# Optimization experiments

Hardware: AMD Instinct MI355X
Metric: run time of the kernel (lower is better)

The kernel has to match this reference:

```python
import jax, jax.numpy as jnp
import numpy as np

B, C, S, D = 16, 32, 64, 512
DFF, E = 2048, 8


def setup_inputs() -> dict:
    key = jax.random.key(0)
    ks = jax.random.split(key, 16)
    std = 0.02
    return {
        'x': jax.random.normal(ks[0], (B, C, S, D), jnp.float32),
        'baseline': jax.random.normal(ks[1], (B, C, S, D), jnp.float32),
        'attnres': jax.random.normal(ks[2], (B, C, S, D), jnp.float32),
        'shared_w1': jax.random.normal(ks[3], (DFF, D), jnp.float32) * std,
        'shared_b1': jnp.zeros((DFF,), jnp.float32),
        'shared_w2': jax.random.normal(ks[4], (D, DFF), jnp.float32) * std,
        'shared_b2': jnp.zeros((D,), jnp.float32),
        'spa_router_w': jax.random.normal(ks[5], (E, 3 * D), jnp.float32) * std,
        'spa_router_b': jnp.zeros((E,), jnp.float32),
        'spe_router_w': jax.random.normal(ks[6], (E, 3 * D), jnp.float32) * std,
        'spe_router_b': jnp.zeros((E,), jnp.float32),
        'spa_w1': jax.random.normal(ks[7], (E, DFF, D), jnp.float32) * std,
        'spa_b1': jnp.zeros((E, DFF), jnp.float32),
        'spa_w2': jax.random.normal(ks[8], (E, D, DFF), jnp.float32) * std,
        'spa_b2': jnp.zeros((E, D), jnp.float32),
        'spe_w1': jax.random.normal(ks[9], (E, DFF, D), jnp.float32) * std,
        'spe_b1': jnp.zeros((E, DFF), jnp.float32),
        'spe_w2': jax.random.normal(ks[10], (E, D, DFF), jnp.float32) * std,
        'spe_b2': jnp.zeros((E, D), jnp.float32),
    }


def _route(feat, rw, rb):
    # feat [B, 3D] -> top-1 expert index [B] and its softmax gate weight [B]
    logits = feat @ rw.T + rb            # [B, E]
    p = jax.nn.softmax(logits, axis=-1)
    idx = jnp.argmax(logits, axis=-1)    # [B]
    w = jnp.take_along_axis(p, idx[:, None], axis=-1)[:, 0]
    return idx, w


def _specialist(xf, idx, w1, b1, w2, b2):
    # xf [B, T, D]; per-sample gather of expert weights then batched FFN
    W1, B1 = w1[idx], b1[idx]            # [B, DFF, D], [B, DFF]
    W2, B2 = w2[idx], b2[idx]            # [B, D, DFF], [B, D]
    h = jax.nn.gelu(jnp.einsum('btd,bfd->btf', xf, W1) + B1[:, None, :])
    return jnp.einsum('btf,bdf->btd', h, W2) + B2[:, None, :]


def reference(x, baseline, attnres, shared_w1, shared_b1, shared_w2, shared_b2,
              spa_router_w, spa_router_b, spe_router_w, spe_router_b,
              spa_w1, spa_b1, spa_w2, spa_b2, spe_w1, spe_b1, spe_w2, spe_b2):
    b, d = x.shape[0], x.shape[-1]
    xf = x.reshape(b, -1, d)  # [B, T, D]
    # sample-level AttnRes router features: [B, 3*d_model]
    feat = jnp.concatenate([
        baseline.mean(axis=(1, 2)),
        attnres.mean(axis=(1, 2)),
        (attnres - baseline).mean(axis=(1, 2)),
    ], axis=-1)
    spa_idx, spa_w = _route(feat, spa_router_w, spa_router_b)
    spe_idx, spe_w = _route(feat, spe_router_w, spe_router_b)
    # shared dense FFN (dropout=0 eval)
    shared = jax.nn.gelu(xf @ shared_w1.T + shared_b1) @ shared_w2.T + shared_b2
    spa_out = _specialist(xf, spa_idx, spa_w1, spa_b1, spa_w2, spa_b2)
    spe_out = _specialist(xf, spe_idx, spe_w1, spe_b1, spe_w2, spe_b2)
    y = shared + spa_w[:, None, None] * spa_out + spe_w[:, None, None] * spe_out
    return y.reshape(x.shape)
```

## Files before the change

kernel.cpp:

```cpp
#include <hip/hip_runtime.h>
#include <cstdint>
#include <cstddef>

#define DEV __device__ __forceinline__

typedef unsigned short u16;
typedef _Float16 f16x8 __attribute__((ext_vector_type(8)));
typedef float f32x4 __attribute__((ext_vector_type(4)));

static constexpr int NB  = 16;
static constexpr int T   = 2048;
static constexpr int D   = 512;
static constexpr int DFF = 2048;
static constexpr int NE  = 8;
static constexpr int FEAT = 3 * D;

#define MFMA16 __builtin_amdgcn_mfma_f32_16x16x32_f16

DEV u16 f2h(float f) {
  _Float16 h = (_Float16)f;
  union { _Float16 h; u16 u; } cv; cv.h = h; return cv.u;
}

DEV float gelu_fast(float x) {
  const float t = x * x;
  const float p = x * fmaf(t, -0.07135481627f, -1.59576912161f);
  return __fdividef(x, 1.0f + __expf(p));
}


__global__ void k_part(const float* __restrict__ base, const float* __restrict__ attn,
                       float* __restrict__ part) {
  const int b = blockIdx.x >> 4, ch = blockIdx.x & 15;
  const int d = threadIdx.x;
  const size_t o = ((size_t)b * T + (size_t)ch * 128) * D + d;
  const float* pb = base + o;
  const float* pa = attn + o;
  float sb = 0.f, sa = 0.f;
  for (int r = 0; r < 128; ++r) { sb += pb[(size_t)r * D]; sa += pa[(size_t)r * D]; }
  part[(b * 16 + ch) * D + d] = sb;
  part[NB * 16 * D + (b * 16 + ch) * D + d] = sa;
}

__global__ void k_feat(const float* __restrict__ part, float* __restrict__ feat) {
  const int b = blockIdx.x, d = threadIdx.x;
  float sb = 0.f, sa = 0.f;
  for (int ch = 0; ch < 16; ++ch) {
    sb += part[(b * 16 + ch) * D + d];
    sa += part[NB * 16 * D + (b * 16 + ch) * D + d];
  }
  sb *= (1.0f / 2048.0f); sa *= (1.0f / 2048.0f);
  feat[b * FEAT + d] = sb;
  feat[b * FEAT + D + d] = sa;
  feat[b * FEAT + 2 * D + d] = sa - sb;
}

__global__ void k_route(const float* __restrict__ feat,
                        const float* __restrict__ rw0, const float* __restrict__ rb0,
                        const float* __restrict__ rw1, const float* __restrict__ rb1,
                        int* __restrict__ idx, float* __restrict__ gate) {
  const int r = blockIdx.x >> 4, b = blockIdx.x & 15;
  const float* rw = (r == 0) ? rw0 : rw1;
  const float* rb = (r == 0) ? rb0 : rb1;
  const int l = threadIdx.x;
  float p[8];
#pragma unroll
  for (int e = 0; e < 8; ++e) p[e] = 0.f;
  const float* f = feat + b * FEAT;
  for (int k = l; k < FEAT; k += 64) {
    const float fv = f[k];
#pragma unroll
    for (int e = 0; e < 8; ++e) p[e] += fv * rw[e * FEAT + k];
  }
#pragma unroll
  for (int off = 32; off >= 1; off >>= 1) {
#pragma unroll
    for (int e = 0; e < 8; ++e) p[e] += __shfl_xor(p[e], off);
  }
  if (l == 0) {
    float best = -1e30f; int bi = 0;
    float lg[8];
#pragma unroll
    for (int e = 0; e < 8; ++e) {
      lg[e] = p[e] + rb[e];
      if (lg[e] > best) { best = lg[e]; bi = e; }
    }
    float s = 0.f;
#pragma unroll
    for (int e = 0; e < 8; ++e) s += expf(lg[e] - best);
    idx[r * 16 + b] = bi;
    gate[r * 16 + b] = 1.0f / s;
  }
}

__global__ void k_btot(const float* __restrict__ b2s, const float* __restrict__ b2a,
                       const float* __restrict__ b2e, const int* __restrict__ idx,
                       const float* __restrict__ gate, float* __restrict__ btot) {
  const int b = blockIdx.x, d = threadIdx.x;
  const int ia = idx[b], ie = idx[16 + b];
  const float ga = gate[b], ge = gate[16 + b];
  btot[b * D + d] = b2s[d] + ga * b2a[ia * D + d] + ge * b2e[ie * D + d];
}

__global__ void k_cast(const float* __restrict__ s, u16* __restrict__ d, long n) {
  const long i = ((long)blockIdx.x * blockDim.x + threadIdx.x) * 4;
  if (i >= n) return;
  const float4 v = *(const float4*)(s + i);
  const unsigned int lo = (unsigned int)f2h(v.x) | ((unsigned int)f2h(v.y) << 16);
  const unsigned int hi = (unsigned int)f2h(v.z) | ((unsigned int)f2h(v.w) << 16);
  *(uint2*)(d + i) = make_uint2(lo, hi);
}


DEV void ld_lds16(const void* g, void* l) {
  __builtin_amdgcn_global_load_lds((const __attribute__((address_space(1))) void*)g,
                                   (__attribute__((address_space(3))) void*)l, 16, 0, 0);
}

template <int NC>
DEV void gemm_pipe(const u16* __restrict__ A, int lda, const u16* __restrict__ B, int ldb,
                   u16* As, u16* Bs, f32x4 (&acc)[8][4]) {
  static_assert(NC >= 4, "pipeline needs >=4 chunks");
  const int tid = threadIdx.x;
  const int lane = tid & 63, wid = tid >> 6;
  const int wr = wid >> 2, wc = wid & 3;

  const int r0 = wid * 32 + (lane >> 2);
  const int r1 = r0 + 16;
  const int cb0 = (lane & 3) ^ ((r0 >> 1) & 3);
  const int cb1 = (lane & 3) ^ ((r1 >> 1) & 3);
  const int ldsO0 = wid * 1024;
  const int ldsO1 = wid * 1024 + 512;
  const u16* gA0 = A + (size_t)r0 * lda + cb0 * 8;
  const u16* gA1 = A + (size_t)r1 * lda + cb1 * 8;
  const u16* gB0 = B + (size_t)r0 * ldb + cb0 * 8;
  const u16* gB1 = B + (size_t)r1 * ldb + cb1 * 8;

  const int kb = lane >> 4;
  int ar[8], br[4];
#pragma unroll
  for (int m = 0; m < 8; ++m) {
    const int R = wr * 128 + m * 16 + (lane & 15);
    ar[m] = R * 64 + ((kb ^ ((R >> 1) & 3)) * 16);
  }
#pragma unroll
  for (int n = 0; n < 4; ++n) {
    const int C = wc * 64 + n * 16 + (lane & 15);
    br[n] = C * 64 + ((kb ^ ((C >> 1) & 3)) * 16);
  }

  {
    const u16 *a0 = gA0, *a1 = gA1, *b0 = gB0, *b1 = gB1;
#pragma unroll
    for (int c = 0; c < 3; ++c) {
      ld_lds16(a0, As + c * 8192 + ldsO0);
      ld_lds16(a1, As + c * 8192 + ldsO1);
      ld_lds16(b0, Bs + c * 8192 + ldsO0);
      ld_lds16(b1, Bs + c * 8192 + ldsO1);
      a0 += 32; a1 += 32; b0 += 32; b1 += 32;
    }
  }
  const u16 *sA0 = gA0 + 96, *sA1 = gA1 + 96, *sB0 = gB0 + 96, *sB1 = gB1 + 96;
  asm volatile("s_waitcnt vmcnt(8)" ::: "memory");
  __builtin_amdgcn_s_barrier();

  for (int ch = 0; ch < NC; ++ch) {
    const char* Asl = (const char*)(As + (ch & 3) * 8192);
    const char* Bsl = (const char*)(Bs + (ch & 3) * 8192);
    const bool st = (ch + 3) < NC;
    const int ssl = (ch + 3) & 3;

    f16x8 av[8], bv0, bv1, bv2, bv3;
#pragma unroll
    for (int m = 0; m < 8; ++m) av[m] = *(const f16x8*)(Asl + ar[m]);
    bv0 = *(const f16x8*)(Bsl + br[0]);
    bv1 = *(const f16x8*)(Bsl + br[1]);
    if (st) {
      ld_lds16(sA0, As + ssl * 8192 + ldsO0);
      ld_lds16(sA1, As + ssl * 8192 + ldsO1);
    }
    __builtin_amdgcn_s_barrier();
    asm volatile("s_waitcnt lgkmcnt(0)" ::: "memory");
    __builtin_amdgcn_s_setprio(1);
#pragma unroll
    for (int m = 0; m < 8; ++m) {
      acc[m][0] = MFMA16(av[m], bv0, acc[m][0], 0, 0, 0);
      acc[m][1] = MFMA16(av[m], bv1, acc[m][1], 0, 0, 0);
    }
    __builtin_amdgcn_s_setprio(0);
    __builtin_amdgcn_s_barrier();

    bv2 = *(const f16x8*)(Bsl + br[2]);
    bv3 = *(const f16x8*)(Bsl + br[3]);
    if (st) {
      ld_lds16(sB0, Bs + ssl * 8192 + ldsO0);
      ld_lds16(sB1, Bs + ssl * 8192 + ldsO1);
    }
    __builtin_amdgcn_s_barrier();
    asm volatile("s_waitcnt lgkmcnt(0)" ::: "memory");
    __builtin_amdgcn_s_setprio(1);
#pragma unroll
    for (int m = 0; m < 8; ++m) {
      acc[m][2] = MFMA16(av[m], bv2, acc[m][2], 0, 0, 0);
      acc[m][3] = MFMA16(av[m], bv3, acc[m][3], 0, 0, 0);
    }
    __builtin_amdgcn_s_setprio(0);
    sA0 += 32; sA1 += 32; sB0 += 32; sB1 += 32;

    if (ch < NC - 3)       asm volatile("s_waitcnt vmcnt(8)" ::: "memory");
    else if (ch == NC - 3) asm volatile("s_waitcnt vmcnt(4)" ::: "memory");
    else if (ch == NC - 2) asm volatile("s_waitcnt vmcnt(0)" ::: "memory");
    __builtin_amdgcn_s_barrier();
  }
}

template <int BANK>
__global__ __launch_bounds__(512, 2) void k_ffn1(
    const u16* __restrict__ xh, const u16* __restrict__ w1, const float* __restrict__ b1,
    const int* __restrict__ idx, const float* __restrict__ gate, u16* __restrict__ h) {
  __shared__ alignas(16) u16 As[4 * 8192];
  __shared__ alignas(16) u16 Bs[4 * 8192];
  int wg = blockIdx.x;
  const int q = (int)gridDim.x >> 3;
  wg = (wg & 7) * q + (wg >> 3);
  const int b  = wg >> 6;
  const int mt = (wg >> 3) & 7;
  const int nt = wg & 7;

  const int e   = (BANK == 0) ? 0 : idx[(BANK - 1) * 16 + b];
  const float g = (BANK == 0) ? 1.0f : gate[(BANK - 1) * 16 + b];
  const u16* Ab = xh + ((size_t)b * T + (size_t)mt * 256) * D;
  const u16* Bb = w1 + (size_t)e * DFF * D + (size_t)nt * 256 * D;
  const float* bb = b1 + (size_t)e * DFF;

  f32x4 acc[8][4];
#pragma unroll
  for (int m = 0; m < 8; ++m)
#pragma unroll
    for (int n = 0; n < 4; ++n)
#pragma unroll
      for (int r = 0; r < 4; ++r) acc[m][n][r] = 0.f;

  gemm_pipe<16>(Ab, D, Bb, D, As, Bs, acc);

  const int lane = threadIdx.x & 63, wid = threadIdx.x >> 6;
  const int wr = wid >> 2, wc = wid & 3;
  const int rr = (lane >> 4) << 2, cc = lane & 15;
  const int mrow = mt * 256 + wr * 128;
  const int ncol = nt * 256 + wc * 64;
  u16* hb = h + (size_t)b * T * DFF;
  float bias[4];
#pragma unroll
  for (int n = 0; n < 4; ++n) bias[n] = bb[ncol + n * 16 + cc];
#pragma unroll
  for (int m = 0; m < 8; ++m) {
    const int row = mrow + m * 16 + rr;
#pragma unroll
    for (int n = 0; n < 4; ++n) {
      const int col = ncol + n * 16 + cc;
      const f32x4 a = acc[m][n];
#pragma unroll
      for (int r = 0; r < 4; ++r) {
        const float v = gelu_fast(a[r] + bias[n]) * g;
        hb[(size_t)(row + r) * DFF + col] = f2h(v);
      }
    }
  }
}

template <int BANK>
__global__ __launch_bounds__(512, 2) void k_ffn2(
    const u16* __restrict__ h, const u16* __restrict__ w2, const float* __restrict__ btot,
    const int* __restrict__ idx, float* __restrict__ out) {
  __shared__ alignas(16) u16 As[4 * 8192];
  __shared__ alignas(16) u16 Bs[4 * 8192];
  int wg = blockIdx.x;
  const int q = (int)gridDim.x >> 3;
  wg = (wg & 7) * q + (wg >> 3);
  const int b  = wg >> 4;
  const int mt = (wg >> 1) & 7;
  const int nt = wg & 1;

  const int e = (BANK == 0) ? 0 : idx[(BANK - 1) * 16 + b];
  const u16* Ab = h + ((size_t)b * T + (size_t)mt * 256) * DFF;
  const u16* Bb = w2 + (size_t)e * D * DFF + (size_t)nt * 256 * DFF;

  f32x4 acc[8][4];
#pragma unroll
  for (int m = 0; m < 8; ++m)
#pragma unroll
    for (int n = 0; n < 4; ++n)
#pragma unroll
      for (int r = 0; r < 4; ++r) acc[m][n][r] = 0.f;

  gemm_pipe<64>(Ab, DFF, Bb, DFF, As, Bs, acc);

  const int lane = threadIdx.x & 63, wid = threadIdx.x >> 6;
  const int wr = wid >> 2, wc = wid & 3;
  const int rr = (lane >> 4) << 2, cc = lane & 15;
  const int mrow = mt * 256 + wr * 128;
  const int ncol = nt * 256 + wc * 64;
  float* ob = out + (size_t)b * T * D;
  float bt[4];
#pragma unroll
  for (int n = 0; n < 4; ++n) bt[n] = btot[b * D + ncol + n * 16 + cc];
#pragma unroll
  for (int m = 0; m < 8; ++m) {
    const int row = mrow + m * 16 + rr;
#pragma unroll
    for (int n = 0; n < 4; ++n) {
      const int col = ncol + n * 16 + cc;
      const f32x4 a = acc[m][n];
#pragma unroll
      for (int r = 0; r < 4; ++r) {
        const size_t oi = (size_t)(row + r) * D + col;
        if (BANK == 0) ob[oi] = a[r] + bt[n];
        else           ob[oi] += a[r];
      }
    }
  }
}


extern "C" void kernel_launch(void* const* d_in, const int* in_sizes, int n_in,
                              void* d_out, int out_size, void* d_ws, size_t ws_size,
                              hipStream_t stream) {
  (void)in_sizes; (void)n_in; (void)out_size; (void)ws_size;
  const float* x    = (const float*)d_in[0];
  const float* base = (const float*)d_in[1];
  const float* attn = (const float*)d_in[2];
  const float* sw1  = (const float*)d_in[3];
  const float* sb1  = (const float*)d_in[4];
  const float* sw2  = (const float*)d_in[5];
  const float* sb2  = (const float*)d_in[6];
  const float* arw  = (const float*)d_in[7];
  const float* arb  = (const float*)d_in[8];
  const float* erw  = (const float*)d_in[9];
  const float* erb  = (const float*)d_in[10];
  const float* aw1  = (const float*)d_in[11];
  const float* ab1  = (const float*)d_in[12];
  const float* aw2  = (const float*)d_in[13];
  const float* ab2  = (const float*)d_in[14];
  const float* ew1  = (const float*)d_in[15];
  const float* eb1  = (const float*)d_in[16];
  const float* ew2  = (const float*)d_in[17];
  const float* eb2  = (const float*)d_in[18];
  float* out = (float*)d_out;

  char* w = (char*)d_ws;
  u16* xh   = (u16*)w;  w += (size_t)NB * T * D * 2;
  u16* hbuf = (u16*)w;  w += (size_t)NB * T * DFF * 2;
  u16* w1s  = (u16*)w;  w += (size_t)DFF * D * 2;
  u16* w2s  = (u16*)w;  w += (size_t)D * DFF * 2;
  u16* w1a  = (u16*)w;  w += (size_t)NE * DFF * D * 2;
  u16* w2a  = (u16*)w;  w += (size_t)NE * D * DFF * 2;
  u16* w1e  = (u16*)w;  w += (size_t)NE * DFF * D * 2;
  u16* w2e  = (u16*)w;  w += (size_t)NE * D * DFF * 2;
  float* part = (float*)w; w += (size_t)2 * NB * 16 * D * 4;
  float* feat = (float*)w; w += (size_t)NB * FEAT * 4;
  int*   idx  = (int*)w;   w += 32 * 4;
  float* gate = (float*)w; w += 32 * 4;
  float* btot = (float*)w; w += (size_t)NB * D * 4;

  k_part<<<dim3(256), dim3(512), 0, stream>>>(base, attn, part);
  k_feat<<<dim3(16), dim3(512), 0, stream>>>(part, feat);
  k_route<<<dim3(32), dim3(64), 0, stream>>>(feat, arw, arb, erw, erb, idx, gate);
  k_btot<<<dim3(16), dim3(512), 0, stream>>>(sb2, ab2, eb2, idx, gate, btot);

  {
    long n;
    n = (long)NB * T * D;      k_cast<<<(unsigned)(n / 1024), 256, 0, stream>>>(x,   xh,  n);
    n = (long)DFF * D;         k_cast<<<(unsigned)(n / 1024), 256, 0, stream>>>(sw1, w1s, n);
    n = (long)D * DFF;         k_cast<<<(unsigned)(n / 1024), 256, 0, stream>>>(sw2, w2s, n);
    n = (long)NE * DFF * D;    k_cast<<<(unsigned)(n / 1024), 256, 0, stream>>>(aw1, w1a, n);
    n = (long)NE * D * DFF;    k_cast<<<(unsigned)(n / 1024), 256, 0, stream>>>(aw2, w2a, n);
    n = (long)NE * DFF * D;    k_cast<<<(unsigned)(n / 1024), 256, 0, stream>>>(ew1, w1e, n);
    n = (long)NE * D * DFF;    k_cast<<<(unsigned)(n / 1024), 256, 0, stream>>>(ew2, w2e, n);
  }

  const dim3 g1(1024), g2(256), blk(512);
  k_ffn1<0><<<g1, blk, 0, stream>>>(xh, w1s, sb1, idx, gate, hbuf);
  k_ffn2<0><<<g2, blk, 0, stream>>>(hbuf, w2s, btot, idx, out);
  k_ffn1<1><<<g1, blk, 0, stream>>>(xh, w1a, ab1, idx, gate, hbuf);
  k_ffn2<1><<<g2, blk, 0, stream>>>(hbuf, w2a, btot, idx, out);
  k_ffn1<2><<<g1, blk, 0, stream>>>(xh, w1e, eb1, idx, gate, hbuf);
  k_ffn2<2><<<g2, blk, 0, stream>>>(hbuf, w2e, btot, idx, out);
}
```

Before: 737.1 us.

## Skip casting unused expert weights and restructure GEMM LDS pipeline

Routing now records which experts are selected in a flag array, and the fp16 cast of expert weight banks skips experts no sample uses, saving memory traffic on unused weights. The GEMM main loop is rewritten to double-buffer the A-fragment registers across chunk pairs, overlapping LDS reads of the next chunk with MFMAs of the current one and cutting barriers per chunk. Launch bounds drop the min-2-blocks hint, letting the compiler use more registers at possible occupancy cost. This adds register pressure and a tiny extra zeroing kernel.

```diff
diff --git a/kernel.cpp b/kernel.cpp
--- a/kernel.cpp
+++ b/kernel.cpp
@@ -55,10 +55,15 @@
   feat[b * FEAT + 2 * D + d] = sa - sb;
 }
 
+__global__ void k_zero(int* __restrict__ used) {
+  used[threadIdx.x] = 0;
+}
+
 __global__ void k_route(const float* __restrict__ feat,
                         const float* __restrict__ rw0, const float* __restrict__ rb0,
                         const float* __restrict__ rw1, const float* __restrict__ rb1,
-                        int* __restrict__ idx, float* __restrict__ gate) {
+                        int* __restrict__ idx, float* __restrict__ gate,
+                        int* __restrict__ used) {
   const int r = blockIdx.x >> 4, b = blockIdx.x & 15;
   const float* rw = (r == 0) ? rw0 : rw1;
   const float* rb = (r == 0) ? rb0 : rb1;
@@ -90,6 +95,7 @@
     for (int e = 0; e < 8; ++e) s += expf(lg[e] - best);
     idx[r * 16 + b] = bi;
     gate[r * 16 + b] = 1.0f / s;
+    atomicOr(&used[r * 8 + bi], 1);
   }
 }
 
@@ -111,6 +117,17 @@
   *(uint2*)(d + i) = make_uint2(lo, hi);
 }
 
+__global__ void k_cast_gated(const float* __restrict__ s, u16* __restrict__ d,
+                             const int* __restrict__ used) {
+  const int e = blockIdx.x >> 10;
+  if (!used[e]) return;
+  const long i = (long)e * (DFF * D) + ((long)(blockIdx.x & 1023) * 256 + threadIdx.x) * 4;
+  const float4 v = *(const float4*)(s + i);
+  const unsigned int lo = (unsigned int)f2h(v.x) | ((unsigned int)f2h(v.y) << 16);
+  const unsigned int hi = (unsigned int)f2h(v.z) | ((unsigned int)f2h(v.w) << 16);
+  *(uint2*)(d + i) = make_uint2(lo, hi);
+}
+
 
 DEV void ld_lds16(const void* g, void* l) {
   __builtin_amdgcn_global_load_lds((const __attribute__((address_space(1))) void*)g,
@@ -120,7 +137,7 @@
 template <int NC>
 DEV void gemm_pipe(const u16* __restrict__ A, int lda, const u16* __restrict__ B, int ldb,
                    u16* As, u16* Bs, f32x4 (&acc)[8][4]) {
-  static_assert(NC >= 4, "pipeline needs >=4 chunks");
+  static_assert(NC >= 4 && (NC % 2) == 0, "NC must be even and >= 4");
   const int tid = threadIdx.x;
   const int lane = tid & 63, wid = tid >> 6;
   const int wr = wid >> 2, wc = wid & 3;
@@ -131,10 +148,10 @@
   const int cb1 = (lane & 3) ^ ((r1 >> 1) & 3);
   const int ldsO0 = wid * 1024;
   const int ldsO1 = wid * 1024 + 512;
-  const u16* gA0 = A + (size_t)r0 * lda + cb0 * 8;
-  const u16* gA1 = A + (size_t)r1 * lda + cb1 * 8;
-  const u16* gB0 = B + (size_t)r0 * ldb + cb0 * 8;
-  const u16* gB1 = B + (size_t)r1 * ldb + cb1 * 8;
+  const u16* pA0 = A + (size_t)r0 * lda + cb0 * 8;
+  const u16* pA1 = A + (size_t)r1 * lda + cb1 * 8;
+  const u16* pB0 = B + (size_t)r0 * ldb + cb0 * 8;
+  const u16* pB1 = B + (size_t)r1 * ldb + cb1 * 8;
 
   const int kb = lane >> 4;
   int ar[8], br[4];
@@ -149,73 +166,70 @@
     br[n] = C * 64 + ((kb ^ ((C >> 1) & 3)) * 16);
   }
 
-  {
-    const u16 *a0 = gA0, *a1 = gA1, *b0 = gB0, *b1 = gB1;
-#pragma unroll
-    for (int c = 0; c < 3; ++c) {
-      ld_lds16(a0, As + c * 8192 + ldsO0);
-      ld_lds16(a1, As + c * 8192 + ldsO1);
-      ld_lds16(b0, Bs + c * 8192 + ldsO0);
-      ld_lds16(b1, Bs + c * 8192 + ldsO1);
-      a0 += 32; a1 += 32; b0 += 32; b1 += 32;
+#define STAGE(c) do { const int sl_ = (c) & 3; const long off_ = (long)(c) * 32;   \
+    ld_lds16(pA0 + off_, As + sl_ * 8192 + ldsO0);                                 \
+    ld_lds16(pA1 + off_, As + sl_ * 8192 + ldsO1);                                 \
+    ld_lds16(pB0 + off_, Bs + sl_ * 8192 + ldsO0);                                 \
+    ld_lds16(pB1 + off_, Bs + sl_ * 8192 + ldsO1); } while (0)
+
+#define RD_A(dst, c) do { const char* sl_ = (const char*)(As + ((c) & 3) * 8192);  \
+    _Pragma("unroll") for (int m_ = 0; m_ < 8; ++m_)                               \
+      dst[m_] = *(const f16x8*)(sl_ + ar[m_]); } while (0)
+
+#define RD_B(c) do { const char* sl_ = (const char*)(Bs + ((c) & 3) * 8192);       \
+    _Pragma("unroll") for (int n_ = 0; n_ < 4; ++n_)                               \
+      bv[n_] = *(const f16x8*)(sl_ + br[n_]); } while (0)
+
+#define MFMA_SET(av) do {                                                          \
+    __builtin_amdgcn_s_setprio(1);                                                 \
+    _Pragma("unroll") for (int m_ = 0; m_ < 8; ++m_) {                             \
+      acc[m_][0] = MFMA16(av[0 + m_], bv[0], acc[m_][0], 0, 0, 0);                 \
+      acc[m_][1] = MFMA16(av[0 + m_], bv[1], acc[m_][1], 0, 0, 0);                 \
+      acc[m_][2] = MFMA16(av[0 + m_], bv[2], acc[m_][2], 0, 0, 0);                 \
+      acc[m_][3] = MFMA16(av[0 + m_], bv[3], acc[m_][3], 0, 0, 0); }               \
+    __builtin_amdgcn_s_setprio(0); } while (0)
+
+  f16x8 avA[8], avB[8], bv[4];
+
+  STAGE(0); STAGE(1); STAGE(2);
+  asm volatile("s_waitcnt vmcnt(4)" ::: "memory");
+  __builtin_amdgcn_s_barrier();
+  RD_A(avA, 0);
+  RD_B(0);
+
+  for (int c = 0; c < NC; c += 2) {
+    {
+      RD_A(avB, c + 1);
+      if (c + 3 < NC) STAGE(c + 3);
+      asm volatile("s_waitcnt lgkmcnt(8)" ::: "memory");
+      MFMA_SET(avA);
+      RD_B(c + 1);
+      if (c + 3 < NC)      asm volatile("s_waitcnt vmcnt(4)" ::: "memory");
+      else if (c + 2 < NC) asm volatile("s_waitcnt vmcnt(0)" ::: "memory");
+      __builtin_amdgcn_s_barrier();
     }
-  }
-  const u16 *sA0 = gA0 + 96, *sA1 = gA1 + 96, *sB0 = gB0 + 96, *sB1 = gB1 + 96;
-  asm volatile("s_waitcnt vmcnt(8)" ::: "memory");
-  __builtin_amdgcn_s_barrier();
-
-  for (int ch = 0; ch < NC; ++ch) {
-    const char* Asl = (const char*)(As + (ch & 3) * 8192);
-    const char* Bsl = (const char*)(Bs + (ch & 3) * 8192);
-    const bool st = (ch + 3) < NC;
-    const int ssl = (ch + 3) & 3;
-
-    f16x8 av[8], bv0, bv1, bv2, bv3;
-#pragma unroll
-    for (int m = 0; m < 8; ++m) av[m] = *(const f16x8*)(Asl + ar[m]);
-    bv0 = *(const f16x8*)(Bsl + br[0]);
-    bv1 = *(const f16x8*)(Bsl + br[1]);
-    if (st) {
-      ld_lds16(sA0, As + ssl * 8192 + ldsO0);
-      ld_lds16(sA1, As + ssl * 8192 + ldsO1);
+    {
+      const int c1 = c + 1;
+      const bool more = (c1 + 1) < NC;
+      if (more) RD_A(avA, c1 + 1);
+      if (c1 + 3 < NC) STAGE(c1 + 3);
+      if (more) asm volatile("s_waitcnt lgkmcnt(8)" ::: "memory");
+      else      asm volatile("s_waitcnt lgkmcnt(0)" ::: "memory");
+      MFMA_SET(avB);
+      if (more) RD_B(c1 + 1);
+      if (c1 + 3 < NC)      asm volatile("s_waitcnt vmcnt(4)" ::: "memory");
+      else if (c1 + 2 < NC) asm volatile("s_waitcnt vmcnt(0)" ::: "memory");
+      __builtin_amdgcn_s_barrier();
     }
-    __builtin_amdgcn_s_barrier();
-    asm volatile("s_waitcnt lgkmcnt(0)" ::: "memory");
-    __builtin_amdgcn_s_setprio(1);
-#pragma unroll
-    for (int m = 0; m < 8; ++m) {
-      acc[m][0] = MFMA16(av[m], bv0, acc[m][0], 0, 0, 0);
-      acc[m][1] = MFMA16(av[m], bv1, acc[m][1], 0, 0, 0);
-    }
-    __builtin_amdgcn_s_setprio(0);
-    __builtin_amdgcn_s_barrier();
-
-    bv2 = *(const f16x8*)(Bsl + br[2]);
-    bv3 = *(const f16x8*)(Bsl + br[3]);
-    if (st) {
-      ld_lds16(sB0, Bs + ssl * 8192 + ldsO0);
-      ld_lds16(sB1, Bs + ssl * 8192 + ldsO1);
-    }
-    __builtin_amdgcn_s_barrier();
-    asm volatile("s_waitcnt lgkmcnt(0)" ::: "memory");
-    __builtin_amdgcn_s_setprio(1);
-#pragma unroll
-    for (int m = 0; m < 8; ++m) {
-      acc[m][2] = MFMA16(av[m], bv2, acc[m][2], 0, 0, 0);
-      acc[m][3] = MFMA16(av[m], bv3, acc[m][3], 0, 0, 0);
-    }
-    __builtin_amdgcn_s_setprio(0);
-    sA0 += 32; sA1 += 32; sB0 += 32; sB1 += 32;
-
-    if (ch < NC - 3)       asm volatile("s_waitcnt vmcnt(8)" ::: "memory");
-    else if (ch == NC - 3) asm volatile("s_waitcnt vmcnt(4)" ::: "memory");
-    else if (ch == NC - 2) asm volatile("s_waitcnt vmcnt(0)" ::: "memory");
-    __builtin_amdgcn_s_barrier();
-  }
+  }
+#undef STAGE
+#undef RD_A
+#undef RD_B
+#undef MFMA_SET
 }
 
 template <int BANK>
-__global__ __launch_bounds__(512, 2) void k_ffn1(
+__global__ __launch_bounds__(512) void k_ffn1(
     const u16* __restrict__ xh, const u16* __restrict__ w1, const float* __restrict__ b1,
     const int* __restrict__ idx, const float* __restrict__ gate, u16* __restrict__ h) {
   __shared__ alignas(16) u16 As[4 * 8192];
@@ -269,7 +283,7 @@
 }
 
 template <int BANK>
-__global__ __launch_bounds__(512, 2) void k_ffn2(
+__global__ __launch_bounds__(512) void k_ffn2(
     const u16* __restrict__ h, const u16* __restrict__ w2, const float* __restrict__ btot,
     const int* __restrict__ idx, float* __restrict__ out) {
   __shared__ alignas(16) u16 As[4 * 8192];
@@ -361,21 +375,23 @@
   int*   idx  = (int*)w;   w += 32 * 4;
   float* gate = (float*)w; w += 32 * 4;
   float* btot = (float*)w; w += (size_t)NB * D * 4;
-
+  int*   used = (int*)w;   w += 16 * 4;
+
+  k_zero<<<dim3(1), dim3(16), 0, stream>>>(used);
   k_part<<<dim3(256), dim3(512), 0, stream>>>(base, attn, part);
   k_feat<<<dim3(16), dim3(512), 0, stream>>>(part, feat);
-  k_route<<<dim3(32), dim3(64), 0, stream>>>(feat, arw, arb, erw, erb, idx, gate);
+  k_route<<<dim3(32), dim3(64), 0, stream>>>(feat, arw, arb, erw, erb, idx, gate, used);
   k_btot<<<dim3(16), dim3(512), 0, stream>>>(sb2, ab2, eb2, idx, gate, btot);
 
   {
     long n;
-    n = (long)NB * T * D;      k_cast<<<(unsigned)(n / 1024), 256, 0, stream>>>(x,   xh,  n);
-    n = (long)DFF * D;         k_cast<<<(unsigned)(n / 1024), 256, 0, stream>>>(sw1, w1s, n);
-    n = (long)D * DFF;         k_cast<<<(unsigned)(n / 1024), 256, 0, stream>>>(sw2, w2s, n);
-    n = (long)NE * DFF * D;    k_cast<<<(unsigned)(n / 1024), 256, 0, stream>>>(aw1, w1a, n);
-    n = (long)NE * D * DFF;    k_cast<<<(unsigned)(n / 1024), 256, 0, stream>>>(aw2, w2a, n);
-    n = (long)NE * DFF * D;    k_cast<<<(unsigned)(n / 1024), 256, 0, stream>>>(ew1, w1e, n);
-    n = (long)NE * D * DFF;    k_cast<<<(unsigned)(n / 1024), 256, 0, stream>>>(ew2, w2e, n);
+    n = (long)NB * T * D;  k_cast<<<(unsigned)(n / 1024), 256, 0, stream>>>(x,   xh,  n);
+    n = (long)DFF * D;     k_cast<<<(unsigned)(n / 1024), 256, 0, stream>>>(sw1, w1s, n);
+    n = (long)D * DFF;     k_cast<<<(unsigned)(n / 1024), 256, 0, stream>>>(sw2, w2s, n);
+    k_cast_gated<<<dim3(8192), 256, 0, stream>>>(aw1, w1a, used);
+    k_cast_gated<<<dim3(8192), 256, 0, stream>>>(aw2, w2a, used);
+    k_cast_gated<<<dim3(8192), 256, 0, stream>>>(ew1, w1e, used + 8);
+    k_cast_gated<<<dim3(8192), 256, 0, stream>>>(ew2, w2e, used + 8);
   }
 
   const dim3 g1(1024), g2(256), blk(512);
```

After: 753.1 us. +2.2%, slower.
